# Kernel optimization log

Hardware: AMD Instinct MI355X
Metric: run time of the kernel (lower is better)

The kernel has to match this reference:

```python
import jax, jax.numpy as jnp
import numpy as np

T = 4
TAU = 2.0      # spikingjelly MultiStepLIFNode default
VTH = 1.0
EPS = 1e-6


def heaviside(x):
    return (x >= 0.0).astype(x.dtype)


def lif_multistep(x_seq):
    """Multi-step LIF over leading time axis. x_seq: [T, ...] -> spikes [T, ...].
    v' = v + (x - v)/tau ; spike = H(v' - vth) ; hard reset to 0 (detach_reset)."""
    def step(v, x):
        v = v + (x - v) / TAU
        s = heaviside(v - VTH)
        v = v * (1.0 - jax.lax.stop_gradient(s))
        return v, s
    _, s_seq = jax.lax.scan(step, jnp.zeros_like(x_seq[0]), x_seq)
    return s_seq


def reference(features, edge_index, W1, b1, W2, b2, fc_W, fc_b):
    N = features.shape[0]
    # GCN normalization with self-loops
    self_idx = jnp.arange(N, dtype=edge_index.dtype)
    src = jnp.concatenate([edge_index[0], self_idx])
    dst = jnp.concatenate([edge_index[1], self_idx])
    deg = jnp.zeros((N,), jnp.float32).at[dst].add(1.0)
    dinv = jax.lax.rsqrt(jnp.maximum(deg, 1.0))
    norm = dinv[src] * dinv[dst]  # [E+N]

    def gcn_conv(x, W, b):
        # x: [T, N, d_in]; aggregation is linear, so aggregate then project
        msg = x[:, src, :] * norm[None, :, None]
        agg = jnp.zeros_like(x).at[:, dst].add(msg)
        return jnp.einsum('tnd,df->tnf', agg, W) + b

    x = jnp.broadcast_to(features, (T,) + features.shape)  # repeat over T steps
    h = lif_multistep(gcn_conv(x, W1, b1))   # [T, N, hidden]
    h = lif_multistep(gcn_conv(h, W2, b2))   # [T, N, embed]
    s = lif_multistep(jnp.einsum('tnd,dc->tnc', h, fc_W) + fc_b)  # [T, N, C]
    return jnp.log(s.sum(0) / T + EPS)       # [N, C]


def setup_inputs() -> dict:
    key = jax.random.key(0)
    ks = jax.random.split(key, 6)
    N, E, D, H, EMB, C = 100000, 1600000, 128, 256, 256, 40
    return {
        'features': jax.random.normal(ks[0], (N, D), jnp.float32),
        'edge_index': jax.random.randint(ks[1], (2, E), 0, N, jnp.int64),
        'W1': jax.random.normal(ks[2], (D, H), jnp.float32) * 0.05,
        'b1': jnp.zeros((H,), jnp.float32),
        'W2': jax.random.normal(ks[3], (H, EMB), jnp.float32) * 0.05,
        'b2': jnp.zeros((EMB,), jnp.float32),
        'fc_W': jax.random.normal(ks[4], (EMB, C), jnp.float32) * 0.05,
        'fc_b': jnp.zeros((C,), jnp.float32),
    }
```

## Files before the change

### kernel.cpp

```cpp
#include <hip/hip_runtime.h>
#include <hip/hip_bf16.h>
#include <math.h>

typedef __attribute__((ext_vector_type(8))) short bf16x8;
typedef __attribute__((ext_vector_type(2))) float floatx2;
typedef __attribute__((ext_vector_type(4))) float floatx4;
typedef __attribute__((ext_vector_type(4))) int intx4;
typedef __attribute__((ext_vector_type(4))) unsigned int uintx4;

#define CAPA 512
#define CAPR 1024
#define CAPE 32768
#define THR_SPIKE (16.0f/15.0f - 1e-4f)

__device__ __forceinline__ float bf2f(unsigned short u){
  union { unsigned int i; float f; } x; x.i = ((unsigned int)u) << 16; return x.f;
}
__device__ __forceinline__ unsigned short f2b(float f){
  union { float f; unsigned int i; } x; x.f = f;
  unsigned int r = x.i + 0x7fffu + ((x.i >> 16) & 1u);
  return (unsigned short)(r >> 16);
}
__device__ __forceinline__ int lif4(float x){
  float v = 0.f; int b = 0;
#pragma unroll
  for (int t = 0; t < 4; ++t){
    v = 0.5f * (v + x);
    if (v >= 1.0f){ b |= (1 << t); v = 0.f; }
  }
  return b;
}

__device__ __forceinline__ void default_row(const float* b2, const float* fcW,
                                            const float* fcb, float* od){
  int lane = threadIdx.x;
  unsigned bits_q[4];
#pragma unroll
  for (int q=0;q<4;++q) bits_q[q] = (unsigned)lif4(b2[lane*4+q]);
  unsigned long long bal[4][4];
  for (int t=0;t<4;++t)
    for (int q=0;q<4;++q)
      bal[t][q] = __ballot((bits_q[q]>>t)&1u);
  if (lane < 40){
    float v = 0.f, cnt = 0.f;
    for (int t=0;t<4;++t){
      float x = fcb[lane];
      for (int q=0;q<4;++q){
        unsigned long long m = bal[t][q];
        while (m){ int l = __ffsll(m)-1; m &= m-1; x += fcW[(size_t)(l*4+q)*40 + lane]; }
      }
      v = 0.5f*(v+x);
      if (v >= 1.f){ cnt += 1.f; v = 0.f; }
    }
    od[lane] = logf(cnt*0.25f + 1e-6f);
  }
}

__global__ void k_count(const int* ei, int E, int N, int aligned4, unsigned* indeg8){
  long long g = (long long)blockIdx.x*256 + threadIdx.x;
  int seg = blockIdx.x & 7;
  long long base = g*8;
  size_t sb = (size_t)seg * (size_t)N;
  if (aligned4 && base + 7 < E){
    intx4 a = *(const intx4*)(ei + E + base);
    intx4 b = *(const intx4*)(ei + E + base + 4);
#pragma unroll
    for (int j=0;j<4;++j) atomicAdd(&indeg8[sb + (unsigned)a[j]], 1u);
#pragma unroll
    for (int j=0;j<4;++j) atomicAdd(&indeg8[sb + (unsigned)b[j]], 1u);
  } else {
    for (long long x = base; x < E && x < base+8; ++x)
      atomicAdd(&indeg8[sb + (unsigned)ei[E + x]], 1u);
  }
}

__global__ void k_redA(const unsigned* v, unsigned* bsum, int M){
  __shared__ unsigned s[256];
  int t = threadIdx.x;
  int i = blockIdx.x*1024 + t*4;
  unsigned a = 0u;
  if (i + 3 < M){ uintx4 u = *(const uintx4*)(v + i); a = u.x+u.y+u.z+u.w; }
  else { for (int j=i;j<M && j<i+4;++j) a += v[j]; }
  s[t] = a; __syncthreads();
  for (int off=128; off>0; off>>=1){
    if (t < off) s[t] += s[t+off];
    __syncthreads();
  }
  if (t == 0) bsum[blockIdx.x] = s[0];
}

__global__ void k_scanTop(const unsigned* bsum, unsigned* boff, int NB, unsigned* totalOut){
  __shared__ unsigned s[512];
  int t = threadIdx.x;
  unsigned carry = 0u;
  for (int base = 0; base < NB; base += 512){
    int i = base + t;
    unsigned a = (i < NB) ? bsum[i] : 0u;
    __syncthreads();
    s[t] = a; __syncthreads();
    for (int off=1; off<512; off<<=1){
      unsigned x = (t>=off) ? s[t-off] : 0u;
      __syncthreads(); s[t] += x; __syncthreads();
    }
    if (i < NB) boff[i] = carry + s[t] - a;
    __syncthreads();
    carry += s[511];
  }
  if (t == 0) *totalOut = carry;
}

__global__ void k_scanLocal(const unsigned* v, const unsigned* boff,
                            unsigned* row, unsigned* cur, int M){
  __shared__ unsigned s[256];
  int t = threadIdx.x;
  int i = blockIdx.x*1024 + t*4;
  unsigned e0=0,e1=0,e2=0,e3=0;
  if (i + 3 < M){ uintx4 u = *(const uintx4*)(v + i); e0=u.x;e1=u.y;e2=u.z;e3=u.w; }
  else if (i < M){ e0=v[i]; if(i+1<M)e1=v[i+1]; if(i+2<M)e2=v[i+2]; if(i+3<M)e3=v[i+3]; }
  unsigned tot = e0+e1+e2+e3;
  s[t] = tot; __syncthreads();
  for (int off=1; off<256; off<<=1){
    unsigned x = (t>=off) ? s[t-off] : 0u;
    __syncthreads(); s[t] += x; __syncthreads();
  }
  unsigned ex = boff[blockIdx.x] + s[t] - tot;
  if (i + 3 < M){
    uintx4 r; r.x = ex; r.y = ex+e0; r.z = ex+e0+e1; r.w = ex+e0+e1+e2;
    *(uintx4*)(row + i) = r;
    *(uintx4*)(cur + i) = r;
  } else {
    unsigned p = ex;
    if (i   < M){ row[i]=p;   cur[i]=p;   p+=e0; }
    if (i+1 < M){ row[i+1]=p; cur[i+1]=p; p+=e1; }
    if (i+2 < M){ row[i+2]=p; cur[i+2]=p; p+=e2; }
    if (i+3 < M){ row[i+3]=p; cur[i+3]=p; }
  }
}

__global__ void k_dinv(const unsigned* indeg8, float* dinv, int N){
  int i = blockIdx.x*256 + threadIdx.x;
  if (i < N){
    unsigned deg = 0u;
#pragma unroll
    for (int s=0;s<8;++s) deg += indeg8[(size_t)s*N + i];
    dinv[i] = rsqrtf((float)(deg + 1u));
  }
}

__global__ void k_fused(const int* ei, int E, int N, int aligned4, int GB8,
                        unsigned* cur8, unsigned* csr_src,
                        const float* feat, const float* dinv, const float* W1,
                        unsigned* gtab8, unsigned short* Wt,
                        const float* b2, const float* fcW, const float* fcb,
                        float* outdef){
  if ((int)blockIdx.x < GB8){
    long long g = (long long)blockIdx.x*256 + threadIdx.x;
    int seg = blockIdx.x & 7;
    long long base = g*8;
    size_t sb = (size_t)seg * (size_t)N;
    if (aligned4 && base + 7 < E){
      intx4 s4a = *(const intx4*)(ei + base);
      intx4 s4b = *(const intx4*)(ei + base + 4);
      intx4 d4a = *(const intx4*)(ei + E + base);
      intx4 d4b = *(const intx4*)(ei + E + base + 4);
#pragma unroll
      for (int j=0;j<4;++j){
        unsigned p = atomicAdd(&cur8[sb + (unsigned)d4a[j]], 1u);
        csr_src[p] = (unsigned)s4a[j];
      }
#pragma unroll
      for (int j=0;j<4;++j){
        unsigned p = atomicAdd(&cur8[sb + (unsigned)d4b[j]], 1u);
        csr_src[p] = (unsigned)s4b[j];
      }
    } else {
      for (long long x = base; x < E && x < base+8; ++x){
        unsigned p = atomicAdd(&cur8[sb + (unsigned)ei[E + x]], 1u);
        csr_src[p] = (unsigned)ei[x];
      }
    }
  } else {
    int bid2 = (int)blockIdx.x - GB8;
    int stride = ((int)gridDim.x - GB8) * 256;
    int tid2 = bid2*256 + threadIdx.x;
    if (bid2 == 0 && threadIdx.x < 64)
      default_row(b2, fcW, fcb, outdef);
    int total4 = N*32;
    for (int i = tid2; i < total4; i += stride){
      floatx4 f = *(const floatx4*)(feat + (size_t)i*4);
      float dv = dinv[i >> 5];
      int w = __builtin_amdgcn_cvt_pk_fp8_f32(f[0]*dv, f[1]*dv, 0, false);
      w     = __builtin_amdgcn_cvt_pk_fp8_f32(f[2]*dv, f[3]*dv, w, true);
      gtab8[i] = (unsigned)w;
    }
    for (int i = tid2; i < 128*256; i += stride){
      int k = i >> 8, c = i & 255; Wt[c*128 + k] = f2b(W1[i]);
    }
  }
}

__global__ void k_agg1(const unsigned char* gtab8, const unsigned* row8,
                       const unsigned* csr_src, const float* dinv,
                       unsigned* aggb, int N){
  int gw = (blockIdx.x*blockDim.x + threadIdx.x) >> 6;
  int lane = threadIdx.x & 63;
  if (gw >= N) return;
  int grp = lane >> 3;
  int lc  = lane & 7;
  unsigned e  = row8[(size_t)grp*N + gw];
  unsigned en = row8[(size_t)grp*N + gw + 1];
  floatx2 acc[8];
#pragma unroll
  for (int k=0;k<8;++k) acc[k] = (floatx2){0.f, 0.f};
  auto acc_add = [&](uintx4 w){
#pragma unroll
    for (int j=0;j<4;++j){
      int word = (int)((j==0)?w.x:(j==1)?w.y:(j==2)?w.z:w.w);
      acc[2*j]   += __builtin_amdgcn_cvt_pk_f32_fp8(word, false);
      acc[2*j+1] += __builtin_amdgcn_cvt_pk_f32_fp8(word, true);
    }
  };
  if (grp == 0){
    uintx4 w = *(const uintx4*)(gtab8 + (size_t)gw*128 + lc*16);
    acc_add(w);
  }
  bool act = e < en;
  unsigned src = act ? csr_src[e] : 0u;
  while (__any(act)){
    uintx4 w = (uintx4){0u,0u,0u,0u};
    if (act) w = *(const uintx4*)(gtab8 + (size_t)src*128 + lc*16);
    unsigned e2 = e + (act ? 1u : 0u);
    bool act2 = e2 < en;
    unsigned src2 = act2 ? csr_src[e2] : 0u;
    if (act) acc_add(w);
    e = e2; act = act2; src = src2;
  }
#pragma unroll
  for (int k=0;k<8;++k){
#pragma unroll
    for (int d=8; d<64; d<<=1){
      acc[k].x += __shfl_xor(acc[k].x, d);
      acc[k].y += __shfl_xor(acc[k].y, d);
    }
  }
  if (grp == 0){
    float dn = dinv[gw];
    unsigned r[8];
#pragma unroll
    for (int k=0;k<8;++k)
      r[k] = (unsigned)f2b(acc[k].x*dn) | ((unsigned)f2b(acc[k].y*dn) << 16);
    unsigned* dst = aggb + (size_t)gw*64 + lc*8;
    *(uintx4*)(dst)     = (uintx4){r[0],r[1],r[2],r[3]};
    *(uintx4*)(dst + 4) = (uintx4){r[4],r[5],r[6],r[7]};
  }
}

__global__ __launch_bounds__(256, 3) void k_gemm1(
    const unsigned short* aggb, const unsigned short* Wt, const float* b1,
    unsigned* ctrs, unsigned* activeA, unsigned* bitmap,
    const float* outdef, float* out, int N, int ntiles){
  __shared__ float od[40];
  if (threadIdx.x < 40) od[threadIdx.x] = outdef[threadIdx.x];
  int wave = threadIdx.x >> 6, lane = threadIdx.x & 63;
  int g = lane >> 4, lc = lane & 15;
  int cg = wave;
  bf16x8 B[4][4];
#pragma unroll
  for (int ct=0; ct<4; ++ct)
#pragma unroll
    for (int kt=0; kt<4; ++kt)
      B[ct][kt] = *(const bf16x8*)(Wt + (size_t)(cg*64 + ct*16 + lc)*128 + kt*32 + g*8);
  float bias[4];
#pragma unroll
  for (int ct=0; ct<4; ++ct) bias[ct] = b1[cg*64 + ct*16 + lc];
  __syncthreads();

  for (int tile = blockIdx.x; tile < ntiles; tile += gridDim.x){
    int row0 = tile*32;
    floatx4 acc[2][4];
#pragma unroll
    for (int rb=0; rb<2; ++rb)
#pragma unroll
      for (int ct=0; ct<4; ++ct) acc[rb][ct] = (floatx4){0.f,0.f,0.f,0.f};
#pragma unroll
    for (int rb=0; rb<2; ++rb){
      int arow = row0 + rb*16 + lc; if (arow >= N) arow = N-1;
#pragma unroll
      for (int kt=0; kt<4; ++kt){
        bf16x8 a = *(const bf16x8*)(aggb + (size_t)arow*128 + kt*32 + g*8);
#pragma unroll
        for (int ct=0; ct<4; ++ct)
          acc[rb][ct] = __builtin_amdgcn_mfma_f32_16x16x32_bf16(a, B[ct][kt], acc[rb][ct], 0,0,0);
      }
    }
#pragma unroll
    for (int rb=0; rb<2; ++rb){
      unsigned pj = 0u;
#pragma unroll
      for (int ct=0; ct<4; ++ct)
#pragma unroll
        for (int j=0; j<4; ++j)
          if (acc[rb][ct][j] + bias[ct] >= THR_SPIKE) pj |= (1u<<j);
      if (__any(pj != 0u)){
#pragma unroll
        for (int j=0; j<4; ++j){
          unsigned long long bal = __ballot((pj>>j)&1u);
          if (lc == 0){
            unsigned m16 = (unsigned)((bal >> (g*16)) & 0xFFFFull);
            int node = row0 + rb*16 + g*4 + j;
            if (m16 && node < N){
              unsigned bit = 1u << (node & 31);
              unsigned old = atomicOr(&bitmap[node >> 5], bit);
              if (!(old & bit)){
                unsigned idx = atomicAdd(&ctrs[0], 1u);
                if (idx < CAPA) activeA[idx] = (unsigned)node;
              }
            }
          }
        }
      }
    }
    int hi = row0 + 32; if (hi > N) hi = N;
    int cnt = (hi - row0) * 40;
    float* obase = out + (size_t)row0 * 40;
    for (int k = threadIdx.x; k < cnt; k += 256) obase[k] = od[k % 40];
  }
}

__global__ void k_fallback(const float* b2, const float* fcW, const float* fcb,
                           float* out, int N){
  __shared__ float od[40];
  if (threadIdx.x < 64) default_row(b2, fcW, fcb, od);
  __syncthreads();
  int total = N*40;
  int stride = gridDim.x*blockDim.x;
  for (int i = blockIdx.x*blockDim.x + threadIdx.x; i < total; i += stride)
    out[i] = od[i % 40];
}

__global__ __launch_bounds__(1024) void k_sparse(
    unsigned* ctrs, const unsigned* activeA, const unsigned short* aggb,
    const float* W1, const float* b1, const float* W2,
    const int* ei, int E, int N, const float* dinv,
    unsigned* map, unsigned* actIdx, unsigned* elist, unsigned* recv,
    float* w2sum, float* a2c,
    const float* b2, const float* fcW, const float* fcb, float* out){
  if (ctrs[0] == 0u) return;
  int tid = threadIdx.x;
  int nA = (int)min(ctrs[0], (unsigned)CAPA);
  __shared__ unsigned se, sr;
  __shared__ float srow[4][128];
  __shared__ unsigned char sbits[4][256];
  if (tid == 0){ se = 0u; sr = 0u; }
  for (int i = tid; i < 4*CAPR*256; i += 1024) a2c[i] = 0.f;
  for (int i = tid; i < N; i += 1024){ map[i] = 0xFFFFFFFFu; actIdx[i] = 0xFFFFFFFFu; }
  __syncthreads();
  int sub = tid >> 8, f = tid & 255;
  int nAp = (nA + 3) & ~3;
  for (int i = sub; i < nAp; i += 4){
    bool on = (i < nA);
    int node = on ? (int)activeA[i] : 0;
    if (on && f == 0) actIdx[node] = (unsigned)i;
    if (on && f < 128) srow[sub][f] = bf2f(aggb[(size_t)node*128 + f]);
    __syncthreads();
    if (on){
      float a = b1[f];
      for (int k=0;k<128;++k) a += srow[sub][k] * W1[k*256 + f];
      sbits[sub][f] = (unsigned char)lif4(a);
    }
    __syncthreads();
    if (on){
      float acc[4] = {0.f,0.f,0.f,0.f};
      for (int b=0;b<256;++b){
        unsigned bits = sbits[sub][b];
        if (bits){
          float wv = W2[(size_t)b*256 + f];
#pragma unroll
          for (int t=0;t<4;++t) if ((bits>>t)&1u) acc[t] += wv;
        }
      }
#pragma unroll
      for (int t=0;t<4;++t) w2sum[((size_t)t*CAPA + i)*256 + f] = acc[t];
    }
    __syncthreads();
  }
  for (int i = tid; i < nA; i += 1024) map[activeA[i]] = 0xFFFFFFFEu;
  for (int e = tid; e < E; e += 1024){
    unsigned s = (unsigned)ei[e];
    if (actIdx[s] != 0xFFFFFFFFu){
      map[(unsigned)ei[E + e]] = 0xFFFFFFFEu;
      unsigned idx = atomicAdd(&se, 1u);
      if (idx < CAPE) elist[idx] = (unsigned)e;
    }
  }
  __syncthreads();
  for (int n = tid; n < N; n += 1024){
    if (map[n] == 0xFFFFFFFEu){
      unsigned slot = atomicAdd(&sr, 1u);
      if (slot < CAPR){ map[n] = slot; recv[slot] = (unsigned)n; }
      else map[n] = 0xFFFFFFFFu;
    }
  }
  __syncthreads();
  int nE = (int)min(se, (unsigned)CAPE);
  for (int j = sub; j < nE + nA; j += 4){
    unsigned i, slot; float nr;
    if (j < nE){
      unsigned e = elist[j];
      unsigned s = (unsigned)ei[e], d = (unsigned)ei[E + e];
      i = actIdx[s]; slot = map[d]; nr = dinv[s]*dinv[d];
    } else {
      unsigned node = activeA[j - nE];
      i = (unsigned)(j - nE); slot = map[node];
      float dn = dinv[node]; nr = dn*dn;
    }
    if (slot < CAPR){
#pragma unroll
      for (int t=0;t<4;++t)
        atomicAdd(&a2c[((size_t)t*CAPR + slot)*256 + f],
                  nr * w2sum[((size_t)t*CAPA + i)*256 + f]);
    }
  }
  __syncthreads();
  int nR = (int)min(sr, (unsigned)CAPR);
  int wv = tid >> 6, lane = tid & 63;
  for (int r = wv; r < nR; r += 16){
    int node = (int)recv[r];
    unsigned bits_q[4];
#pragma unroll
    for (int q=0;q<4;++q){
      int ff = lane*4+q;
      float v = 0.f; unsigned b=0;
      float bb = b2[ff];
#pragma unroll
      for (int t=0;t<4;++t){
        float x = atomicAdd(&a2c[((size_t)t*CAPR + r)*256 + ff], 0.f) + bb;
        v = 0.5f*(v+x);
        if (v>=1.f){ b |= 1u<<t; v=0.f; }
      }
      bits_q[q]=b;
    }
    unsigned long long bal[4][4];
    for (int t=0;t<4;++t)
      for (int q=0;q<4;++q)
        bal[t][q]=__ballot((bits_q[q]>>t)&1u);
    if (lane < 40){
      float v=0.f, cnt=0.f;
      for (int t=0;t<4;++t){
        float x = fcb[lane];
        for (int q=0;q<4;++q){
          unsigned long long m = bal[t][q];
          while (m){ int l=__ffsll(m)-1; m&=m-1; x += fcW[(size_t)(l*4+q)*40 + lane]; }
        }
        v=0.5f*(v+x);
        if (v>=1.f){cnt+=1.f; v=0.f;}
      }
      out[(size_t)node*40 + lane] = logf(cnt*0.25f + 1e-6f);
    }
  }
}

extern "C" void kernel_launch(void* const* d_in, const int* in_sizes, int n_in,
                              void* d_out, int out_size, void* d_ws, size_t ws_size,
                              hipStream_t stream) {
  const float* features = (const float*)d_in[0];
  const int*   ei       = (const int*)d_in[1];
  const float* W1       = (const float*)d_in[2];
  const float* b1       = (const float*)d_in[3];
  const float* W2       = (const float*)d_in[4];
  const float* b2       = (const float*)d_in[5];
  const float* fcW      = (const float*)d_in[6];
  const float* fcb      = (const float*)d_in[7];
  float* out = (float*)d_out;

  const int N  = in_sizes[0] / 128;
  const int E  = in_sizes[1] / 2;
  const int M8 = N * 8;
  const int NB8 = (M8 + 1023) / 1024;
  const int NBo = (N + 255) / 256;
  const int GB8 = (E + 2047) / 2048;
  const int aligned4 = ((E & 3) == 0) ? 1 : 0;
  const int ntiles = (N + 31) / 32;
  (void)n_in; (void)out_size;

  char* w = (char*)d_ws;
  size_t off = 0;
  auto alloc = [&](size_t bytes)->char*{
    char* p = w + off; off += (bytes + 255) & ~(size_t)255; return p;
  };
  unsigned* indeg8  = (unsigned*)alloc((size_t)M8*4);
  unsigned* ctrs    = (unsigned*)alloc(64);
  unsigned* bitmap  = (unsigned*)alloc(((size_t)(N+31)/32)*4);
  size_t msSpan = off;
  unsigned* cur8    = (unsigned*)alloc((size_t)M8*4);
  unsigned* row8    = (unsigned*)alloc(((size_t)M8+1)*4);
  unsigned* bsum8   = (unsigned*)alloc((size_t)NB8*4);
  unsigned* boff8   = (unsigned*)alloc((size_t)NB8*4);
  float*    dinv    = (float*)   alloc((size_t)N*4);
  size_t spNeed = ((size_t)4*CAPA*256 + (size_t)4*CAPR*256) * 4;
  size_t csrBytes = (size_t)E*4; if (csrBytes < spNeed) csrBytes = spNeed;
  char*     csrReg  = alloc(csrBytes);
  unsigned* csr_src = (unsigned*)csrReg;
  float*    w2sum   = (float*)csrReg;
  float*    a2c     = (float*)(csrReg + (size_t)4*CAPA*256*4);
  unsigned* gtab8   = (unsigned*)alloc((size_t)N*128);
  unsigned short* Wt   = (unsigned short*)alloc((size_t)128*256*2);
  unsigned short* aggb = (unsigned short*)alloc((size_t)N*128*2);
  unsigned* activeA = (unsigned*)alloc((size_t)CAPA*4);
  unsigned* recv    = (unsigned*)alloc((size_t)CAPR*4);
  unsigned* map     = (unsigned*)alloc((size_t)N*4);
  unsigned* actIdx  = (unsigned*)alloc((size_t)N*4);
  unsigned* elist   = (unsigned*)alloc((size_t)CAPE*4);
  float*    outdef  = (float*)   alloc(64*4);

  if (off > ws_size){
    k_fallback<<<2048, 256, 0, stream>>>(b2, fcW, fcb, out, N);
    return;
  }

  hipMemsetAsync(d_ws, 0, msSpan, stream);
  k_count     <<<GB8, 256, 0, stream>>>(ei, E, N, aligned4, indeg8);
  k_redA      <<<NB8, 256, 0, stream>>>(indeg8, bsum8, M8);
  k_scanTop   <<<1,  512, 0, stream>>>(bsum8, boff8, NB8, &row8[M8]);
  k_scanLocal <<<NB8, 256, 0, stream>>>(indeg8, boff8, row8, cur8, M8);
  k_dinv      <<<NBo, 256, 0, stream>>>(indeg8, dinv, N);
  k_fused     <<<GB8 + 2048, 256, 0, stream>>>(ei, E, N, aligned4, GB8,
                                               cur8, csr_src,
                                               features, dinv, W1, gtab8, Wt,
                                               b2, fcW, fcb, outdef);
  k_agg1      <<<(N+3)/4, 256, 0, stream>>>((const unsigned char*)gtab8, row8, csr_src,
                                            dinv, (unsigned*)aggb, N);
  k_gemm1     <<<1024, 256, 0, stream>>>(aggb, Wt, b1, ctrs, activeA, bitmap,
                                         outdef, out, N, ntiles);
  k_sparse    <<<1, 1024, 0, stream>>>(ctrs, activeA, aggb, W1, b1, W2,
                                       ei, E, N, dinv, map, actIdx, elist, recv,
                                       w2sum, a2c, b2, fcW, fcb, out);
}
```

Measured before the change: 260.6 us.

## Replace three-pass CSR offset scan with single-pass decoupled look-back scan

```diff
diff --git a/kernel.cpp b/kernel.cpp
--- a/kernel.cpp
+++ b/kernel.cpp
@@ -74,56 +74,58 @@
   }
 }
 
-__global__ void k_redA(const unsigned* v, unsigned* bsum, int M){
+__global__ void k_scan(const unsigned* v, unsigned* row, unsigned* cur,
+                       unsigned long long* desc, int M, int NB){
   __shared__ unsigned s[256];
-  int t = threadIdx.x;
-  int i = blockIdx.x*1024 + t*4;
-  unsigned a = 0u;
-  if (i + 3 < M){ uintx4 u = *(const uintx4*)(v + i); a = u.x+u.y+u.z+u.w; }
-  else { for (int j=i;j<M && j<i+4;++j) a += v[j]; }
-  s[t] = a; __syncthreads();
-  for (int off=128; off>0; off>>=1){
-    if (t < off) s[t] += s[t+off];
-    __syncthreads();
-  }
-  if (t == 0) bsum[blockIdx.x] = s[0];
-}
-
-__global__ void k_scanTop(const unsigned* bsum, unsigned* boff, int NB, unsigned* totalOut){
-  __shared__ unsigned s[512];
-  int t = threadIdx.x;
-  unsigned carry = 0u;
-  for (int base = 0; base < NB; base += 512){
-    int i = base + t;
-    unsigned a = (i < NB) ? bsum[i] : 0u;
-    __syncthreads();
-    s[t] = a; __syncthreads();
-    for (int off=1; off<512; off<<=1){
-      unsigned x = (t>=off) ? s[t-off] : 0u;
-      __syncthreads(); s[t] += x; __syncthreads();
-    }
-    if (i < NB) boff[i] = carry + s[t] - a;
-    __syncthreads();
-    carry += s[511];
-  }
-  if (t == 0) *totalOut = carry;
-}
-
-__global__ void k_scanLocal(const unsigned* v, const unsigned* boff,
-                            unsigned* row, unsigned* cur, int M){
-  __shared__ unsigned s[256];
-  int t = threadIdx.x;
-  int i = blockIdx.x*1024 + t*4;
+  __shared__ unsigned sbase;
+  int b = blockIdx.x, t = threadIdx.x;
+  int i = b*1024 + t*4;
   unsigned e0=0,e1=0,e2=0,e3=0;
   if (i + 3 < M){ uintx4 u = *(const uintx4*)(v + i); e0=u.x;e1=u.y;e2=u.z;e3=u.w; }
-  else if (i < M){ e0=v[i]; if(i+1<M)e1=v[i+1]; if(i+2<M)e2=v[i+2]; if(i+3<M)e3=v[i+3]; }
+  else if (i < M){ e0=v[i]; if(i+1<M)e1=v[i+1]; if(i+2<M)e2=v[i+2]; }
   unsigned tot = e0+e1+e2+e3;
   s[t] = tot; __syncthreads();
   for (int off=1; off<256; off<<=1){
     unsigned x = (t>=off) ? s[t-off] : 0u;
     __syncthreads(); s[t] += x; __syncthreads();
   }
-  unsigned ex = boff[blockIdx.x] + s[t] - tot;
+  unsigned blkSum = s[255];
+  if (b == 0){
+    if (t == 0){
+      atomicExch(&desc[0], (2ull<<32) | (unsigned long long)blkSum);
+      sbase = 0u;
+    }
+  } else if (t < 64){
+    if (t == 0) atomicExch(&desc[b], (1ull<<32) | (unsigned long long)blkSum);
+    unsigned run = 0; int base = b-1;
+    for (;;){
+      int j = base - t;
+      unsigned long long d = 0ull; unsigned f = 0u;
+      if (j >= 0){
+        do { d = atomicAdd(&desc[j], 0ull); f = (unsigned)(d>>32); } while (f == 0u);
+      }
+      unsigned long long preMask = __ballot(j >= 0 && f == 2u);
+      unsigned val = (unsigned)d;
+      if (preMask){
+        int firstPre = __ffsll((long long)preMask) - 1;
+        unsigned contrib = (t < firstPre) ? val : (t == firstPre ? val : 0u);
+#pragma unroll
+        for (int o=1;o<64;o<<=1) contrib += __shfl_xor(contrib, o);
+        run += contrib; break;
+      } else {
+        unsigned contrib = (j >= 0) ? val : 0u;
+#pragma unroll
+        for (int o=1;o<64;o<<=1) contrib += __shfl_xor(contrib, o);
+        run += contrib; base -= 64;
+      }
+    }
+    if (t == 0){
+      sbase = run;
+      atomicExch(&desc[b], (2ull<<32) | (unsigned long long)(run + blkSum));
+    }
+  }
+  __syncthreads();
+  unsigned ex = sbase + s[t] - tot;
   if (i + 3 < M){
     uintx4 r; r.x = ex; r.y = ex+e0; r.z = ex+e0+e1; r.w = ex+e0+e1+e2;
     *(uintx4*)(row + i) = r;
@@ -132,9 +134,9 @@
     unsigned p = ex;
     if (i   < M){ row[i]=p;   cur[i]=p;   p+=e0; }
     if (i+1 < M){ row[i+1]=p; cur[i+1]=p; p+=e1; }
-    if (i+2 < M){ row[i+2]=p; cur[i+2]=p; p+=e2; }
-    if (i+3 < M){ row[i+3]=p; cur[i+3]=p; }
-  }
+    if (i+2 < M){ row[i+2]=p; cur[i+2]=p; }
+  }
+  if (b == NB-1 && t == 255) row[M] = sbase + blkSum;
 }
 
 __global__ void k_dinv(const unsigned* indeg8, float* dinv, int N){
@@ -147,54 +149,51 @@
   }
 }
 
-__global__ void k_fused(const int* ei, int E, int N, int aligned4, int GB8,
-                        unsigned* cur8, unsigned* csr_src,
-                        const float* feat, const float* dinv, const float* W1,
-                        unsigned* gtab8, unsigned short* Wt,
-                        const float* b2, const float* fcW, const float* fcb,
-                        float* outdef){
-  if ((int)blockIdx.x < GB8){
-    long long g = (long long)blockIdx.x*256 + threadIdx.x;
-    int seg = blockIdx.x & 7;
-    long long base = g*8;
-    size_t sb = (size_t)seg * (size_t)N;
-    if (aligned4 && base + 7 < E){
-      intx4 s4a = *(const intx4*)(ei + base);
-      intx4 s4b = *(const intx4*)(ei + base + 4);
-      intx4 d4a = *(const intx4*)(ei + E + base);
-      intx4 d4b = *(const intx4*)(ei + E + base + 4);
-#pragma unroll
-      for (int j=0;j<4;++j){
-        unsigned p = atomicAdd(&cur8[sb + (unsigned)d4a[j]], 1u);
-        csr_src[p] = (unsigned)s4a[j];
-      }
-#pragma unroll
-      for (int j=0;j<4;++j){
-        unsigned p = atomicAdd(&cur8[sb + (unsigned)d4b[j]], 1u);
-        csr_src[p] = (unsigned)s4b[j];
-      }
-    } else {
-      for (long long x = base; x < E && x < base+8; ++x){
-        unsigned p = atomicAdd(&cur8[sb + (unsigned)ei[E + x]], 1u);
-        csr_src[p] = (unsigned)ei[x];
-      }
+__global__ void k_cvt(const float* feat, const float* dinv, const float* W1,
+                      unsigned* gtab8, unsigned short* Wt, int N,
+                      const float* b2, const float* fcW, const float* fcb,
+                      float* outdef){
+  if (blockIdx.x == 0 && threadIdx.x < 64)
+    default_row(b2, fcW, fcb, outdef);
+  int stride = gridDim.x*blockDim.x;
+  int total4 = N*32;
+  for (int i = blockIdx.x*blockDim.x + threadIdx.x; i < total4; i += stride){
+    floatx4 f = *(const floatx4*)(feat + (size_t)i*4);
+    float dv = dinv[i >> 5];
+    int w = __builtin_amdgcn_cvt_pk_fp8_f32(f[0]*dv, f[1]*dv, 0, false);
+    w     = __builtin_amdgcn_cvt_pk_fp8_f32(f[2]*dv, f[3]*dv, w, true);
+    gtab8[i] = (unsigned)w;
+  }
+  for (int i = blockIdx.x*blockDim.x + threadIdx.x; i < 128*256; i += stride){
+    int k = i >> 8, c = i & 255; Wt[c*128 + k] = f2b(W1[i]);
+  }
+}
+
+__global__ void k_scatter_in(const int* ei, int E, int N, int aligned4,
+                             unsigned* cur8, unsigned* csr_src){
+  long long g = (long long)blockIdx.x*256 + threadIdx.x;
+  int seg = blockIdx.x & 7;
+  long long base = g*8;
+  size_t sb = (size_t)seg * (size_t)N;
+  if (aligned4 && base + 7 < E){
+    intx4 s4a = *(const intx4*)(ei + base);
+    intx4 s4b = *(const intx4*)(ei + base + 4);
+    intx4 d4a = *(const intx4*)(ei + E + base);
+    intx4 d4b = *(const intx4*)(ei + E + base + 4);
+#pragma unroll
+    for (int j=0;j<4;++j){
+      unsigned p = atomicAdd(&cur8[sb + (unsigned)d4a[j]], 1u);
+      csr_src[p] = (unsigned)s4a[j];
+    }
+#pragma unroll
+    for (int j=0;j<4;++j){
+      unsigned p = atomicAdd(&cur8[sb + (unsigned)d4b[j]], 1u);
+      csr_src[p] = (unsigned)s4b[j];
     }
   } else {
-    int bid2 = (int)blockIdx.x - GB8;
-    int stride = ((int)gridDim.x - GB8) * 256;
-    int tid2 = bid2*256 + threadIdx.x;
-    if (bid2 == 0 && threadIdx.x < 64)
-      default_row(b2, fcW, fcb, outdef);
-    int total4 = N*32;
-    for (int i = tid2; i < total4; i += stride){
-      floatx4 f = *(const floatx4*)(feat + (size_t)i*4);
-      float dv = dinv[i >> 5];
-      int w = __builtin_amdgcn_cvt_pk_fp8_f32(f[0]*dv, f[1]*dv, 0, false);
-      w     = __builtin_amdgcn_cvt_pk_fp8_f32(f[2]*dv, f[3]*dv, w, true);
-      gtab8[i] = (unsigned)w;
-    }
-    for (int i = tid2; i < 128*256; i += stride){
-      int k = i >> 8, c = i & 255; Wt[c*128 + k] = f2b(W1[i]);
+    for (long long x = base; x < E && x < base+8; ++x){
+      unsigned p = atomicAdd(&cur8[sb + (unsigned)ei[E + x]], 1u);
+      csr_src[p] = (unsigned)ei[x];
     }
   }
 }
@@ -491,11 +490,10 @@
   unsigned* indeg8  = (unsigned*)alloc((size_t)M8*4);
   unsigned* ctrs    = (unsigned*)alloc(64);
   unsigned* bitmap  = (unsigned*)alloc(((size_t)(N+31)/32)*4);
+  unsigned long long* desc = (unsigned long long*)alloc((size_t)NB8*8);
   size_t msSpan = off;
   unsigned* cur8    = (unsigned*)alloc((size_t)M8*4);
   unsigned* row8    = (unsigned*)alloc(((size_t)M8+1)*4);
-  unsigned* bsum8   = (unsigned*)alloc((size_t)NB8*4);
-  unsigned* boff8   = (unsigned*)alloc((size_t)NB8*4);
   float*    dinv    = (float*)   alloc((size_t)N*4);
   size_t spNeed = ((size_t)4*CAPA*256 + (size_t)4*CAPR*256) * 4;
   size_t csrBytes = (size_t)E*4; if (csrBytes < spNeed) csrBytes = spNeed;
@@ -520,14 +518,11 @@
 
   hipMemsetAsync(d_ws, 0, msSpan, stream);
   k_count     <<<GB8, 256, 0, stream>>>(ei, E, N, aligned4, indeg8);
-  k_redA      <<<NB8, 256, 0, stream>>>(indeg8, bsum8, M8);
-  k_scanTop   <<<1,  512, 0, stream>>>(bsum8, boff8, NB8, &row8[M8]);
-  k_scanLocal <<<NB8, 256, 0, stream>>>(indeg8, boff8, row8, cur8, M8);
+  k_scan      <<<NB8, 256, 0, stream>>>(indeg8, row8, cur8, desc, M8, NB8);
   k_dinv      <<<NBo, 256, 0, stream>>>(indeg8, dinv, N);
-  k_fused     <<<GB8 + 2048, 256, 0, stream>>>(ei, E, N, aligned4, GB8,
-                                               cur8, csr_src,
-                                               features, dinv, W1, gtab8, Wt,
-                                               b2, fcW, fcb, outdef);
+  k_cvt       <<<2048, 256, 0, stream>>>(features, dinv, W1, gtab8, Wt, N,
+                                         b2, fcW, fcb, outdef);
+  k_scatter_in<<<GB8, 256, 0, stream>>>(ei, E, N, aligned4, cur8, csr_src);
   k_agg1      <<<(N+3)/4, 256, 0, stream>>>((const unsigned char*)gtab8, row8, csr_src,
                                             dinv, (unsigned*)aggb, N);
   k_gemm1     <<<1024, 256, 0, stream>>>(aggb, Wt, b1, ctrs, activeA, bitmap,
```

Result: no change. 263.8 us (+1.2%).
